# Performance work log

Hardware: AMD Instinct MI355X
Metric: run time of the kernel (lower is better)

## Reference

```python
import jax, jax.numpy as jnp
import numpy as np

B = 1024          # batch of graphs
NG = 978          # genes (nodes) per graph, hard-coded in the module
E = 20_480_000    # total edges across the batch (~20k per graph)
N = B * NG        # flattened node count


def setup_inputs() -> dict:
    key = jax.random.key(0)
    ks = jax.random.split(key, 14)
    s1 = lambda k, sh, f=0.02: jax.random.normal(k, sh, jnp.float32) * f
    return {
        "input1": jax.random.normal(ks[0], (B, NG), jnp.float32),
        "input2": jax.random.normal(ks[1], (B, NG), jnp.float32),
        "edges": jax.random.randint(ks[2], (2, E), 0, N, jnp.int32),
        "input_others": jax.random.normal(ks[3], (B, 4), jnp.float32),
        # GCNConv(1,1): scalar weight + scalar bias
        "gcn_w": jax.random.normal(ks[4], (), jnp.float32),
        "gcn_b": jnp.zeros((), jnp.float32),
        # encoder fc: 978 -> 2048 -> 100
        "fc1_w": s1(ks[5], (NG, 2048)),
        "fc1_b": jnp.zeros((2048,), jnp.float32),
        "fc2_w": s1(ks[6], (2048, 100)),
        "fc2_b": jnp.zeros((100,), jnp.float32),
        # predictor mlp: 5 -> 4 -> 2
        "mlp1_w": s1(ks[7], (5, 4), 0.3),
        "mlp1_b": jnp.zeros((4,), jnp.float32),
        "mlp2_w": s1(ks[8], (4, 2), 0.3),
        "mlp2_b": jnp.zeros((2,), jnp.float32),
    }


def _encoder(x, edges, gcn_w, gcn_b, fc1_w, fc1_b, fc2_w, fc2_b):
    # x: (B, NG) scalar node features -> flatten to (N,)
    xf = x.reshape(-1)
    # GCNConv(1,1, add_self_loops=False, normalize=False):
    # out[dst] = sum_{(src,dst) in E} w * x[src]  (then + bias on every node)
    msg = xf[edges[0]] * gcn_w                                   # gather (E,)
    agg = jax.ops.segment_sum(msg, edges[1], num_segments=N)     # scatter-add (N,)
    h = (agg + gcn_b).reshape(B, NG)
    h = jax.nn.relu(h)                        # dropout = identity (eval mode)
    h = jax.nn.relu(h @ fc1_w + fc1_b)        # (B, 2048)
    return h @ fc2_w + fc2_b                  # (B, 100)


def _get_r2(a, b):
    a = a - jnp.mean(a, axis=1, keepdims=True)
    b = b - jnp.mean(b, axis=1, keepdims=True)
    num = jnp.sum(a * b, axis=1)
    den = jnp.sqrt(jnp.sum(a * a, axis=1)) * jnp.sqrt(jnp.sum(b * b, axis=1))
    return ((num / den) ** 2)[:, None]        # (B, 1)


def reference(input1, input2, edges, input_others, gcn_w, gcn_b,
              fc1_w, fc1_b, fc2_w, fc2_b, mlp1_w, mlp1_b, mlp2_w, mlp2_b):
    o1 = _encoder(input1, edges, gcn_w, gcn_b, fc1_w, fc1_b, fc2_w, fc2_b)
    o2 = _encoder(input2, edges, gcn_w, gcn_b, fc1_w, fc1_b, fc2_w, fc2_b)
    z = jnp.concatenate([_get_r2(o1, o2), input_others], axis=1)  # (B, 5)
    z = jax.nn.relu(z @ mlp1_w + mlp1_b)
    return z @ mlp2_w + mlp2_b                # (B, 2)
```

## Files before the change

### kernel.cpp

```cpp
#include <hip/hip_runtime.h>

#define NG 978
#define BATCH 1024
#define MR 2048
#define KPAD 1024
#define NEDGES 20480000
#define NNODES (BATCH * NG)
#define N1 2048
#define N2 100
#define NBKT 978
#define BCAP 24576
#define SCHUNK 8192

#define OFF_AGG 0
#define OFF_C2  (OFF_AGG + MR * KPAD)
#define OFF_CUR (OFF_C2 + MR * N2)
#define OFF_XI  (OFF_CUR + 1024)
#define OFF_C1  (OFF_XI + 2 * NNODES)
#define OFF_AGGN (OFF_C1 + MR * N1)
#define OFF_BKT (OFF_AGGN + 2 * NNODES)
#define OFF_END (OFF_BKT + NBKT * BCAP)
#define NEED_BYTES ((size_t)OFF_END * 4)

__global__ __launch_bounds__(256) void k_interleave(const float* __restrict__ x1,
                                                    const float* __restrict__ x2,
                                                    float* __restrict__ xi) {
    int i = blockIdx.x * 256 + threadIdx.x;
    if (i >= NNODES / 4) return;
    float4 a = reinterpret_cast<const float4*>(x1)[i];
    float4 b = reinterpret_cast<const float4*>(x2)[i];
    float4 lo = make_float4(a.x, b.x, a.y, b.y);
    float4 hi = make_float4(a.z, b.z, a.w, b.w);
    reinterpret_cast<float4*>(xi)[2 * i + 0] = lo;
    reinterpret_cast<float4*>(xi)[2 * i + 1] = hi;
}

__global__ __launch_bounds__(256) void k_scatter(const int* __restrict__ edges,
                                                 int* __restrict__ cursor,
                                                 unsigned* __restrict__ bkt) {
    __shared__ int cnt[1024];
    __shared__ int loff[1024];
    __shared__ int gbase[1024];
    __shared__ unsigned sdata[SCHUNK];
    __shared__ unsigned short sbid[SCHUNK];
    __shared__ int wsum[4];

    const int t = threadIdx.x;
    const int lane = t & 63, wid = t >> 6;
    const int chunk = blockIdx.x * SCHUNK;
    const int4* d4 = reinterpret_cast<const int4*>(edges + NEDGES + chunk);
    const int4* s4 = reinterpret_cast<const int4*>(edges + chunk);

    for (int i = t; i < 1024; i += 256) cnt[i] = 0;
    __syncthreads();

#pragma unroll
    for (int j = 0; j < SCHUNK / 1024; ++j) {
        int4 d = d4[t + j * 256];
        atomicAdd(&cnt[d.x >> 10], 1);
        atomicAdd(&cnt[d.y >> 10], 1);
        atomicAdd(&cnt[d.z >> 10], 1);
        atomicAdd(&cnt[d.w >> 10], 1);
    }
    __syncthreads();

    {
        int b0 = t * 4;
        int c0 = cnt[b0], c1 = cnt[b0 + 1], c2 = cnt[b0 + 2], c3 = cnt[b0 + 3];
        int s = c0 + c1 + c2 + c3;
        int x = s;
#pragma unroll
        for (int o = 1; o < 64; o <<= 1) {
            int y = __shfl_up(x, o, 64);
            if (lane >= o) x += y;
        }
        if (lane == 63) wsum[wid] = x;
        __syncthreads();
        int wpre = 0;
        for (int w = 0; w < wid; ++w) wpre += wsum[w];
        int e0 = wpre + x - s;
        int l0 = e0, l1 = e0 + c0, l2 = l1 + c1, l3 = l2 + c2;
        loff[b0] = l0; loff[b0 + 1] = l1; loff[b0 + 2] = l2; loff[b0 + 3] = l3;
        int lb;
        lb = c0 ? atomicAdd(&cursor[b0], c0) : 0;
        gbase[b0] = b0 * BCAP + lb - l0;
        lb = c1 ? atomicAdd(&cursor[b0 + 1], c1) : 0;
        gbase[b0 + 1] = (b0 + 1) * BCAP + lb - l1;
        lb = c2 ? atomicAdd(&cursor[b0 + 2], c2) : 0;
        gbase[b0 + 2] = (b0 + 2) * BCAP + lb - l2;
        lb = c3 ? atomicAdd(&cursor[b0 + 3], c3) : 0;
        gbase[b0 + 3] = (b0 + 3) * BCAP + lb - l3;
    }
    __syncthreads();

#pragma unroll
    for (int j = 0; j < SCHUNK / 1024; ++j) {
        int4 d = d4[t + j * 256];
        int4 s = s4[t + j * 256];
        int dd[4] = {d.x, d.y, d.z, d.w};
        int ss[4] = {s.x, s.y, s.z, s.w};
#pragma unroll
        for (int u = 0; u < 4; ++u) {
            int b = dd[u] >> 10;
            int pos = atomicAdd(&loff[b], 1);
            sdata[pos] = ((unsigned)ss[u] << 10) | (unsigned)(dd[u] & 1023);
            sbid[pos] = (unsigned short)b;
        }
    }
    __syncthreads();

#pragma unroll 4
    for (int e = t; e < SCHUNK; e += 256) {
        int bid = sbid[e];
        int idx = gbase[bid] + e;
        unsigned slot = (unsigned)(idx - bid * BCAP);
        if (slot < BCAP)
            bkt[idx] = sdata[e];
    }
}

__global__ __launch_bounds__(256) void k_accum(const unsigned* __restrict__ bkt,
                                               const int* __restrict__ cursor,
                                               const float* __restrict__ xi,
                                               float* __restrict__ aggN) {
    __shared__ float accX[1024];
    __shared__ float accY[1024];
    const int b = blockIdx.x >> 2;
    const int q = blockIdx.x & 3;
    const int t = threadIdx.x;
    for (int i = t; i < 1024; i += 256) { accX[i] = 0.f; accY[i] = 0.f; }
    __syncthreads();
    const int n = cursor[b];
    const int lo = (n * q) >> 2;
    const int hi = (n * (q + 1)) >> 2;
    const unsigned* bp = bkt + (size_t)b * BCAP;
    const float2* xi2 = reinterpret_cast<const float2*>(xi);
    int i = lo + t;
    for (; i + 256 < hi; i += 512) {
        unsigned p0 = bp[i];
        unsigned p1 = bp[i + 256];
        float2 v0 = xi2[p0 >> 10];
        float2 v1 = xi2[p1 >> 10];
        atomicAdd(&accX[p0 & 1023], v0.x);
        atomicAdd(&accY[p0 & 1023], v0.y);
        atomicAdd(&accX[p1 & 1023], v1.x);
        atomicAdd(&accY[p1 & 1023], v1.y);
    }
    if (i < hi) {
        unsigned p0 = bp[i];
        float2 v0 = xi2[p0 >> 10];
        atomicAdd(&accX[p0 & 1023], v0.x);
        atomicAdd(&accY[p0 & 1023], v0.y);
    }
    __syncthreads();
    float* o = aggN + ((size_t)b << 11);
    for (int j = t; j < 1024; j += 256) {
        atomicAdd(o + 2 * j + 0, accX[j]);
        atomicAdd(o + 2 * j + 1, accY[j]);
    }
}

__global__ __launch_bounds__(256) void k_reshape(const float* __restrict__ aggN,
                                                 float* __restrict__ agg) {
    int idx = blockIdx.x * 256 + threadIdx.x;
    int row = idx >> 8;
    int c4 = (idx & 255) << 2;
    const float2* a2 = reinterpret_cast<const float2*>(aggN);
    float4 vx = make_float4(0.f, 0.f, 0.f, 0.f);
    float4 vy = make_float4(0.f, 0.f, 0.f, 0.f);
    float* px = &vx.x;
    float* py = &vy.x;
#pragma unroll
    for (int u = 0; u < 4; ++u) {
        int col = c4 + u;
        if (col < NG) {
            float2 v = a2[(size_t)row * NG + col];
            px[u] = v.x;
            py[u] = v.y;
        }
    }
    *reinterpret_cast<float4*>(&agg[(size_t)row * KPAD + c4]) = vx;
    *reinterpret_cast<float4*>(&agg[(size_t)(BATCH + row) * KPAD + c4]) = vy;
}

__global__ __launch_bounds__(256) void k_edges(const int* __restrict__ edges,
                                               const float* __restrict__ xi,
                                               float* __restrict__ agg) {
    int t = blockIdx.x * 256 + threadIdx.x;
    int e = t * 4;
    const int4 s4 = *reinterpret_cast<const int4*>(edges + e);
    const int4 d4 = *reinterpret_cast<const int4*>(edges + NEDGES + e);
    int ss[4] = {s4.x, s4.y, s4.z, s4.w};
    int dd[4] = {d4.x, d4.y, d4.z, d4.w};
#pragma unroll
    for (int j = 0; j < 4; ++j) {
        int s = ss[j];
        int d = dd[j];
        float2 xv = *reinterpret_cast<const float2*>(xi + 2 * (size_t)s);
        int row = d / NG;
        int col = d - row * NG;
        float* p = agg + (size_t)row * KPAD + col;
        atomicAdd(p, xv.x);
        atomicAdd(p + (size_t)BATCH * KPAD, xv.y);
    }
}

__global__ __launch_bounds__(512) void k_gemm1(const float* __restrict__ agg,
                                               const float* __restrict__ W,
                                               const float* __restrict__ bias,
                                               const float* __restrict__ gwp,
                                               const float* __restrict__ gbp,
                                               float* __restrict__ C1) {
    __shared__ float As[16][132];
    __shared__ float Bs[16][132];
    const int tid = threadIdx.x;
    const int bm = blockIdx.y * 128;
    const int bn = blockIdx.x * 128;
    const float gw = gwp[0], gb = gbp[0];
    const int rt = tid >> 4;
    const int ct = tid & 15;

    float acc[4][8] = {};

    for (int k0 = 0; k0 < NG; k0 += 16) {
        {
            int r = tid >> 2;
            int k4 = (tid & 3) << 2;
            float4 v = *reinterpret_cast<const float4*>(agg + (size_t)(bm + r) * KPAD + k0 + k4);
            v.x = fmaxf(v.x * gw + gb, 0.f);
            v.y = fmaxf(v.y * gw + gb, 0.f);
            v.z = fmaxf(v.z * gw + gb, 0.f);
            v.w = fmaxf(v.w * gw + gb, 0.f);
            As[k4 + 0][r] = v.x;
            As[k4 + 1][r] = v.y;
            As[k4 + 2][r] = v.z;
            As[k4 + 3][r] = v.w;
        }
        {
            int row = tid >> 5;
            int c4 = (tid & 31) << 2;
            int gk = k0 + row;
            float4 v = make_float4(0.f, 0.f, 0.f, 0.f);
            if (gk < NG) v = *reinterpret_cast<const float4*>(W + (size_t)gk * N1 + bn + c4);
            int pc = c4 + ((c4 >> 6) << 2);
            *reinterpret_cast<float4*>(&Bs[row][pc]) = v;
        }
        __syncthreads();
#pragma unroll
        for (int kk = 0; kk < 16; ++kk) {
            float4 a0 = *reinterpret_cast<const float4*>(&As[kk][rt * 4]);
            int cb = ct * 8;
            int pc = cb + ((cb >> 6) << 2);
            float4 b0 = *reinterpret_cast<const float4*>(&Bs[kk][pc]);
            float4 b1 = *reinterpret_cast<const float4*>(&Bs[kk][pc + 4]);
            float a[4] = {a0.x, a0.y, a0.z, a0.w};
            float b[8] = {b0.x, b0.y, b0.z, b0.w, b1.x, b1.y, b1.z, b1.w};
#pragma unroll
            for (int i2 = 0; i2 < 4; ++i2)
#pragma unroll
                for (int j2 = 0; j2 < 8; ++j2)
                    acc[i2][j2] = fmaf(a[i2], b[j2], acc[i2][j2]);
        }
        __syncthreads();
    }
    const int cbase = bn + ct * 8;
    float4 bb0 = *reinterpret_cast<const float4*>(&bias[cbase]);
    float4 bb1 = *reinterpret_cast<const float4*>(&bias[cbase + 4]);
    float bz[8] = {bb0.x, bb0.y, bb0.z, bb0.w, bb1.x, bb1.y, bb1.z, bb1.w};
#pragma unroll
    for (int i2 = 0; i2 < 4; ++i2) {
        int row = bm + rt * 4 + i2;
        float4 o0, o1;
        o0.x = fmaxf(acc[i2][0] + bz[0], 0.f);
        o0.y = fmaxf(acc[i2][1] + bz[1], 0.f);
        o0.z = fmaxf(acc[i2][2] + bz[2], 0.f);
        o0.w = fmaxf(acc[i2][3] + bz[3], 0.f);
        o1.x = fmaxf(acc[i2][4] + bz[4], 0.f);
        o1.y = fmaxf(acc[i2][5] + bz[5], 0.f);
        o1.z = fmaxf(acc[i2][6] + bz[6], 0.f);
        o1.w = fmaxf(acc[i2][7] + bz[7], 0.f);
        *reinterpret_cast<float4*>(&C1[(size_t)row * N1 + cbase]) = o0;
        *reinterpret_cast<float4*>(&C1[(size_t)row * N1 + cbase + 4]) = o1;
    }
}

__global__ __launch_bounds__(256) void k_gemm2(const float* __restrict__ C1,
                                               const float* __restrict__ W,
                                               float* __restrict__ C2) {
    __shared__ float As[16][68];
    __shared__ float Bs[16][132];
    const int tid = threadIdx.x;
    const int bm = blockIdx.x * 64;
    const int k_base = blockIdx.y * 256;
    const int rt = tid >> 5;
    const int ct = tid & 31;
    float acc[8][4] = {};

    for (int k0 = k_base; k0 < k_base + 256; k0 += 16) {
        {
            int r = tid >> 2;
            int k4 = (tid & 3) << 2;
            float4 v = *reinterpret_cast<const float4*>(C1 + (size_t)(bm + r) * N1 + k0 + k4);
            As[k4 + 0][r] = v.x;
            As[k4 + 1][r] = v.y;
            As[k4 + 2][r] = v.z;
            As[k4 + 3][r] = v.w;
        }
#pragma unroll
        for (int h = 0; h < 2; ++h) {
            int i = tid + h * 256;
            if (i < 400) {
                int kk = i / 25;
                int c4 = (i % 25) * 4;
                *reinterpret_cast<float4*>(&Bs[kk][c4]) =
                    *reinterpret_cast<const float4*>(W + (size_t)(k0 + kk) * N2 + c4);
            }
        }
        __syncthreads();
        int cc = (ct < 25) ? ct * 4 : 100;
#pragma unroll
        for (int kk = 0; kk < 16; ++kk) {
            float4 a0 = *reinterpret_cast<const float4*>(&As[kk][rt * 8]);
            float4 a1 = *reinterpret_cast<const float4*>(&As[kk][rt * 8 + 4]);
            float4 b = *reinterpret_cast<const float4*>(&Bs[kk][cc]);
            float a[8] = {a0.x, a0.y, a0.z, a0.w, a1.x, a1.y, a1.z, a1.w};
#pragma unroll
            for (int i2 = 0; i2 < 8; ++i2) {
                acc[i2][0] = fmaf(a[i2], b.x, acc[i2][0]);
                acc[i2][1] = fmaf(a[i2], b.y, acc[i2][1]);
                acc[i2][2] = fmaf(a[i2], b.z, acc[i2][2]);
                acc[i2][3] = fmaf(a[i2], b.w, acc[i2][3]);
            }
        }
        __syncthreads();
    }
    if (ct < 25) {
#pragma unroll
        for (int i2 = 0; i2 < 8; ++i2) {
            float* p = C2 + (size_t)(bm + rt * 8 + i2) * N2 + ct * 4;
            atomicAdd(p + 0, acc[i2][0]);
            atomicAdd(p + 1, acc[i2][1]);
            atomicAdd(p + 2, acc[i2][2]);
            atomicAdd(p + 3, acc[i2][3]);
        }
    }
}

__global__ __launch_bounds__(64) void k_r2mlp(const float* __restrict__ C2,
                                              const float* __restrict__ fc2b,
                                              const float* __restrict__ others,
                                              const float* __restrict__ m1w,
                                              const float* __restrict__ m1b,
                                              const float* __restrict__ m2w,
                                              const float* __restrict__ m2b,
                                              float* __restrict__ out) {
    const int b = blockIdx.x;
    const int t = threadIdx.x;
    float v1a, v2a, v1b = 0.f, v2b = 0.f;
    {
        float bb = fc2b[t];
        v1a = C2[(size_t)b * N2 + t] + bb;
        v2a = C2[(size_t)(b + BATCH) * N2 + t] + bb;
    }
    const bool sec = (t + 64) < N2;
    if (sec) {
        float bb = fc2b[t + 64];
        v1b = C2[(size_t)b * N2 + t + 64] + bb;
        v2b = C2[(size_t)(b + BATCH) * N2 + t + 64] + bb;
    }
    float s1 = v1a + v1b, s2 = v2a + v2b;
#pragma unroll
    for (int o = 32; o; o >>= 1) {
        s1 += __shfl_xor(s1, o, 64);
        s2 += __shfl_xor(s2, o, 64);
    }
    const float inv = 1.0f / (float)N2;
    float m1 = s1 * inv, m2 = s2 * inv;
    float c1a = v1a - m1, c2a = v2a - m2;
    float c1b = sec ? v1b - m1 : 0.f, c2b = sec ? v2b - m2 : 0.f;
    float num = c1a * c2a + c1b * c2b;
    float d1 = c1a * c1a + c1b * c1b;
    float d2 = c2a * c2a + c2b * c2b;
#pragma unroll
    for (int o = 32; o; o >>= 1) {
        num += __shfl_xor(num, o, 64);
        d1 += __shfl_xor(d1, o, 64);
        d2 += __shfl_xor(d2, o, 64);
    }
    if (t == 0) {
        float r = num / (sqrtf(d1) * sqrtf(d2));
        float r2 = r * r;
        float z[5] = {r2, others[b * 4 + 0], others[b * 4 + 1], others[b * 4 + 2], others[b * 4 + 3]};
        float h[4];
#pragma unroll
        for (int j = 0; j < 4; ++j) {
            float a = m1b[j];
#pragma unroll
            for (int i = 0; i < 5; ++i) a = fmaf(z[i], m1w[i * 4 + j], a);
            h[j] = fmaxf(a, 0.f);
        }
#pragma unroll
        for (int o = 0; o < 2; ++o) {
            float a = m2b[o];
#pragma unroll
            for (int j = 0; j < 4; ++j) a = fmaf(h[j], m2w[j * 2 + o], a);
            out[b * 2 + o] = a;
        }
    }
}

extern "C" void kernel_launch(void* const* d_in, const int* in_sizes, int n_in,
                              void* d_out, int out_size, void* d_ws, size_t ws_size,
                              hipStream_t stream) {
    const float* x1    = (const float*)d_in[0];
    const float* x2    = (const float*)d_in[1];
    const int*   edges = (const int*)d_in[2];
    const float* oth   = (const float*)d_in[3];
    const float* gw    = (const float*)d_in[4];
    const float* gb    = (const float*)d_in[5];
    const float* fc1w  = (const float*)d_in[6];
    const float* fc1b  = (const float*)d_in[7];
    const float* fc2w  = (const float*)d_in[8];
    const float* fc2b  = (const float*)d_in[9];
    const float* m1w   = (const float*)d_in[10];
    const float* m1b   = (const float*)d_in[11];
    const float* m2w   = (const float*)d_in[12];
    const float* m2b   = (const float*)d_in[13];

    float* ws   = (float*)d_ws;
    float* agg  = ws + OFF_AGG;
    float* C2   = ws + OFF_C2;
    int*   cur  = (int*)(ws + OFF_CUR);
    float* xi   = ws + OFF_XI;
    float* C1   = ws + OFF_C1;
    float* aggN = ws + OFF_AGGN;
    unsigned* bkt = (unsigned*)(ws + OFF_BKT);
    float* out = (float*)d_out;

    k_interleave<<<(NNODES / 4 + 255) / 256, 256, 0, stream>>>(x1, x2, xi);

    if (ws_size >= NEED_BYTES) {
        hipMemsetAsync(C2, 0, (size_t)(MR * N2 + 1024) * sizeof(float), stream);
        hipMemsetAsync(aggN, 0, (size_t)(2 * NNODES) * sizeof(float), stream);
        k_scatter<<<NEDGES / SCHUNK, 256, 0, stream>>>(edges, cur, bkt);
        k_accum<<<NBKT * 4, 256, 0, stream>>>(bkt, cur, xi, aggN);
        k_reshape<<<BATCH * (KPAD / 4) / 256, 256, 0, stream>>>(aggN, agg);
    } else {
        hipMemsetAsync(agg, 0, (size_t)(MR * KPAD + MR * N2) * sizeof(float), stream);
        k_edges<<<NEDGES / 4 / 256, 256, 0, stream>>>(edges, xi, agg);
    }

    k_gemm1<<<dim3(16, 16), 512, 0, stream>>>(agg, fc1w, fc1b, gw, gb, C1);
    k_gemm2<<<dim3(32, 8), 256, 0, stream>>>(C1, fc2w, C2);
    k_r2mlp<<<1024, 64, 0, stream>>>(C2, fc2b, oth, m1w, m1b, m2w, m2b, out);
}
```

Before: 875.1 us.

## Register-cache edges in scatter, binary-search bucket ids, write accum partials to planes

The scatter kernel now runs 512 threads, loads each edge chunk into registers once instead of reading destinations twice from global memory, and drops the per-edge bucket-id shared array in favour of a binary search over local bucket offsets. The accumulate kernel splits each bucket into two halves that write plain stores into two separate planes, which removes the global float atomics and the aggN memset. The reshape step sums the two planes, and the planes reuse the C1 buffer. This cuts global traffic and atomics, at the cost of a 10-step shared-memory binary search per edge and fewer accumulate blocks.

After: 765.0 us. 12.6% less time.

```diff
diff --git a/kernel.cpp b/kernel.cpp
--- a/kernel.cpp
+++ b/kernel.cpp
@@ -11,6 +11,7 @@
 #define NBKT 978
 #define BCAP 24576
 #define SCHUNK 8192
+#define PLANE (2 * NNODES)
 
 #define OFF_AGG 0
 #define OFF_C2  (OFF_AGG + MR * KPAD)
@@ -35,15 +36,15 @@
     reinterpret_cast<float4*>(xi)[2 * i + 1] = hi;
 }
 
-__global__ __launch_bounds__(256) void k_scatter(const int* __restrict__ edges,
+__global__ __launch_bounds__(512) void k_scatter(const int* __restrict__ edges,
                                                  int* __restrict__ cursor,
                                                  unsigned* __restrict__ bkt) {
     __shared__ int cnt[1024];
+    __shared__ int l0[1024];
     __shared__ int loff[1024];
     __shared__ int gbase[1024];
     __shared__ unsigned sdata[SCHUNK];
-    __shared__ unsigned short sbid[SCHUNK];
-    __shared__ int wsum[4];
+    __shared__ int wsum[8];
 
     const int t = threadIdx.x;
     const int lane = t & 63, wid = t >> 6;
@@ -51,23 +52,29 @@
     const int4* d4 = reinterpret_cast<const int4*>(edges + NEDGES + chunk);
     const int4* s4 = reinterpret_cast<const int4*>(edges + chunk);
 
-    for (int i = t; i < 1024; i += 256) cnt[i] = 0;
-    __syncthreads();
-
-#pragma unroll
-    for (int j = 0; j < SCHUNK / 1024; ++j) {
-        int4 d = d4[t + j * 256];
-        atomicAdd(&cnt[d.x >> 10], 1);
-        atomicAdd(&cnt[d.y >> 10], 1);
-        atomicAdd(&cnt[d.z >> 10], 1);
-        atomicAdd(&cnt[d.w >> 10], 1);
+    for (int i = t; i < 1024; i += 512) cnt[i] = 0;
+
+    int4 dreg[4], sreg[4];
+#pragma unroll
+    for (int j = 0; j < 4; ++j) {
+        dreg[j] = d4[t + j * 512];
+        sreg[j] = s4[t + j * 512];
+    }
+    __syncthreads();
+
+#pragma unroll
+    for (int j = 0; j < 4; ++j) {
+        atomicAdd(&cnt[dreg[j].x >> 10], 1);
+        atomicAdd(&cnt[dreg[j].y >> 10], 1);
+        atomicAdd(&cnt[dreg[j].z >> 10], 1);
+        atomicAdd(&cnt[dreg[j].w >> 10], 1);
     }
     __syncthreads();
 
     {
-        int b0 = t * 4;
-        int c0 = cnt[b0], c1 = cnt[b0 + 1], c2 = cnt[b0 + 2], c3 = cnt[b0 + 3];
-        int s = c0 + c1 + c2 + c3;
+        int b0 = t * 2;
+        int c0 = cnt[b0], c1 = cnt[b0 + 1];
+        int s = c0 + c1;
         int x = s;
 #pragma unroll
         for (int o = 1; o < 64; o <<= 1) {
@@ -79,60 +86,58 @@
         int wpre = 0;
         for (int w = 0; w < wid; ++w) wpre += wsum[w];
         int e0 = wpre + x - s;
-        int l0 = e0, l1 = e0 + c0, l2 = l1 + c1, l3 = l2 + c2;
-        loff[b0] = l0; loff[b0 + 1] = l1; loff[b0 + 2] = l2; loff[b0 + 3] = l3;
+        l0[b0] = e0;       l0[b0 + 1] = e0 + c0;
+        loff[b0] = e0;     loff[b0 + 1] = e0 + c0;
         int lb;
         lb = c0 ? atomicAdd(&cursor[b0], c0) : 0;
-        gbase[b0] = b0 * BCAP + lb - l0;
+        gbase[b0] = lb - e0;
         lb = c1 ? atomicAdd(&cursor[b0 + 1], c1) : 0;
-        gbase[b0 + 1] = (b0 + 1) * BCAP + lb - l1;
-        lb = c2 ? atomicAdd(&cursor[b0 + 2], c2) : 0;
-        gbase[b0 + 2] = (b0 + 2) * BCAP + lb - l2;
-        lb = c3 ? atomicAdd(&cursor[b0 + 3], c3) : 0;
-        gbase[b0 + 3] = (b0 + 3) * BCAP + lb - l3;
-    }
-    __syncthreads();
-
-#pragma unroll
-    for (int j = 0; j < SCHUNK / 1024; ++j) {
-        int4 d = d4[t + j * 256];
-        int4 s = s4[t + j * 256];
-        int dd[4] = {d.x, d.y, d.z, d.w};
-        int ss[4] = {s.x, s.y, s.z, s.w};
+        gbase[b0 + 1] = lb - (e0 + c0);
+    }
+    __syncthreads();
+
+#pragma unroll
+    for (int j = 0; j < 4; ++j) {
+        int dd[4] = {dreg[j].x, dreg[j].y, dreg[j].z, dreg[j].w};
+        int ss[4] = {sreg[j].x, sreg[j].y, sreg[j].z, sreg[j].w};
 #pragma unroll
         for (int u = 0; u < 4; ++u) {
             int b = dd[u] >> 10;
             int pos = atomicAdd(&loff[b], 1);
             sdata[pos] = ((unsigned)ss[u] << 10) | (unsigned)(dd[u] & 1023);
-            sbid[pos] = (unsigned short)b;
         }
     }
     __syncthreads();
 
 #pragma unroll 4
-    for (int e = t; e < SCHUNK; e += 256) {
-        int bid = sbid[e];
-        int idx = gbase[bid] + e;
-        unsigned slot = (unsigned)(idx - bid * BCAP);
+    for (int e = t; e < SCHUNK; e += 512) {
+        unsigned w = sdata[e];
+        int b = 0;
+#pragma unroll
+        for (int step = 512; step >= 1; step >>= 1) {
+            int nb = b + step;
+            if (nb < 1024 && l0[nb] <= e) b = nb;
+        }
+        unsigned slot = (unsigned)(gbase[b] + e);
         if (slot < BCAP)
-            bkt[idx] = sdata[e];
+            bkt[(size_t)b * BCAP + slot] = w;
     }
 }
 
 __global__ __launch_bounds__(256) void k_accum(const unsigned* __restrict__ bkt,
                                                const int* __restrict__ cursor,
                                                const float* __restrict__ xi,
-                                               float* __restrict__ aggN) {
+                                               float* __restrict__ planes) {
     __shared__ float accX[1024];
     __shared__ float accY[1024];
-    const int b = blockIdx.x >> 2;
-    const int q = blockIdx.x & 3;
+    const int b = blockIdx.x >> 1;
+    const int h = blockIdx.x & 1;
     const int t = threadIdx.x;
     for (int i = t; i < 1024; i += 256) { accX[i] = 0.f; accY[i] = 0.f; }
     __syncthreads();
     const int n = cursor[b];
-    const int lo = (n * q) >> 2;
-    const int hi = (n * (q + 1)) >> 2;
+    const int lo = h ? (n >> 1) : 0;
+    const int hi = h ? n : (n >> 1);
     const unsigned* bp = bkt + (size_t)b * BCAP;
     const float2* xi2 = reinterpret_cast<const float2*>(xi);
     int i = lo + t;
@@ -153,19 +158,17 @@
         atomicAdd(&accY[p0 & 1023], v0.y);
     }
     __syncthreads();
-    float* o = aggN + ((size_t)b << 11);
-    for (int j = t; j < 1024; j += 256) {
-        atomicAdd(o + 2 * j + 0, accX[j]);
-        atomicAdd(o + 2 * j + 1, accY[j]);
-    }
-}
-
-__global__ __launch_bounds__(256) void k_reshape(const float* __restrict__ aggN,
+    float2* o = reinterpret_cast<float2*>(planes + (size_t)h * PLANE) + ((size_t)b << 10);
+    for (int j = t; j < 1024; j += 256) o[j] = make_float2(accX[j], accY[j]);
+}
+
+__global__ __launch_bounds__(256) void k_reshape(const float* __restrict__ planes,
                                                  float* __restrict__ agg) {
     int idx = blockIdx.x * 256 + threadIdx.x;
     int row = idx >> 8;
     int c4 = (idx & 255) << 2;
-    const float2* a2 = reinterpret_cast<const float2*>(aggN);
+    const float2* p0 = reinterpret_cast<const float2*>(planes);
+    const float2* p1 = reinterpret_cast<const float2*>(planes + PLANE);
     float4 vx = make_float4(0.f, 0.f, 0.f, 0.f);
     float4 vy = make_float4(0.f, 0.f, 0.f, 0.f);
     float* px = &vx.x;
@@ -174,9 +177,11 @@
     for (int u = 0; u < 4; ++u) {
         int col = c4 + u;
         if (col < NG) {
-            float2 v = a2[(size_t)row * NG + col];
-            px[u] = v.x;
-            py[u] = v.y;
+            size_t ni = (size_t)row * NG + col;
+            float2 a = p0[ni];
+            float2 b = p1[ni];
+            px[u] = a.x + b.x;
+            py[u] = a.y + b.y;
         }
     }
     *reinterpret_cast<float4*>(&agg[(size_t)row * KPAD + c4]) = vx;
@@ -433,7 +438,7 @@
     int*   cur  = (int*)(ws + OFF_CUR);
     float* xi   = ws + OFF_XI;
     float* C1   = ws + OFF_C1;
-    float* aggN = ws + OFF_AGGN;
+    float* planes = C1;
     unsigned* bkt = (unsigned*)(ws + OFF_BKT);
     float* out = (float*)d_out;
 
@@ -441,10 +446,9 @@
 
     if (ws_size >= NEED_BYTES) {
         hipMemsetAsync(C2, 0, (size_t)(MR * N2 + 1024) * sizeof(float), stream);
-        hipMemsetAsync(aggN, 0, (size_t)(2 * NNODES) * sizeof(float), stream);
-        k_scatter<<<NEDGES / SCHUNK, 256, 0, stream>>>(edges, cur, bkt);
-        k_accum<<<NBKT * 4, 256, 0, stream>>>(bkt, cur, xi, aggN);
-        k_reshape<<<BATCH * (KPAD / 4) / 256, 256, 0, stream>>>(aggN, agg);
+        k_scatter<<<NEDGES / SCHUNK, 512, 0, stream>>>(edges, cur, bkt);
+        k_accum<<<NBKT * 2, 256, 0, stream>>>(bkt, cur, xi, planes);
+        k_reshape<<<BATCH * (KPAD / 4) / 256, 256, 0, stream>>>(planes, agg);
     } else {
         hipMemsetAsync(agg, 0, (size_t)(MR * KPAD + MR * N2) * sizeof(float), stream);
         k_edges<<<NEDGES / 4 / 256, 256, 0, stream>>>(edges, xi, agg);
```
